# Kernel tuning notes

Hardware: AMD Instinct MI355X
Metric: run time of the kernel (lower is better)

The kernel has to match this reference:

```python
import jax, jax.numpy as jnp
import numpy as np

N = 100_000      # nodes
E = 3_000_000    # edges
G = 256          # graphs in batch
F_IN = 64        # num_features
NHID = 32


def setup_inputs() -> dict:
    key = jax.random.key(0)
    ks = jax.random.split(key, 12)
    x = jax.random.normal(ks[0], (N, F_IN), dtype=jnp.float32)
    edge_index = jax.random.randint(ks[1], (2, E), 0, N, dtype=jnp.int32)
    batch = jnp.sort(jax.random.randint(ks[2], (N,), 0, G, dtype=jnp.int32))
    # disjoint edge partitions used as integer index arrays (as in the torch code)
    perm = jax.random.permutation(ks[3], E).astype(jnp.int32)
    third = E // 3
    known_mask = perm[:third]
    unk_mask = perm[third:2 * third]
    obs_mask = perm[2 * third:]
    msg_weights = jax.random.normal(ks[4], (3,), dtype=jnp.float32)
    emb_W = jax.random.normal(ks[5], (F_IN - 1, 63), dtype=jnp.float32) * 0.1
    emb_b = jnp.zeros((63,), jnp.float32)
    gcn_W = jax.random.normal(ks[6], (64, NHID), dtype=jnp.float32) * 0.1
    gcn_b = jnp.zeros((NHID,), jnp.float32)
    fc1_W = jax.random.normal(ks[7], (NHID, NHID), dtype=jnp.float32) * 0.1
    fc1_b = jnp.zeros((NHID,), jnp.float32)
    out_W = jax.random.normal(ks[8], (NHID, 1), dtype=jnp.float32) * 0.1
    out_b = jnp.zeros((1,), jnp.float32)
    return dict(x=x, edge_index=edge_index, batch=batch, known_mask=known_mask,
                unk_mask=unk_mask, obs_mask=obs_mask, msg_weights=msg_weights,
                emb_W=emb_W, emb_b=emb_b, gcn_W=gcn_W, gcn_b=gcn_b,
                fc1_W=fc1_W, fc1_b=fc1_b, out_W=out_W, out_b=out_b)


def reference(x, edge_index, batch, known_mask, unk_mask, obs_mask,
              msg_weights, emb_W, emb_b, gcn_W, gcn_b,
              fc1_W, fc1_b, out_W, out_b):
    n_nodes = x.shape[0]
    n_edges = edge_index.shape[1]
    # edge weights from softmaxed message-type params (disjoint index sets)
    sp = jax.nn.softmax(msg_weights)
    ew = jnp.ones((n_edges,), x.dtype)
    ew = ew.at[known_mask].set(sp[0]).at[unk_mask].set(sp[1]).at[obs_mask].set(sp[2])
    # feature embed: keep col 0, embed the remaining 63 -> 63, concat to 64
    h = jnp.concatenate([x[:, :1], x[:, 1:] @ emb_W + emb_b], axis=1)  # [N,64]
    # GCNConv: add self-loops (weight 1), symmetric normalization
    loops = jnp.arange(n_nodes, dtype=edge_index.dtype)
    row = jnp.concatenate([edge_index[0], loops])
    col = jnp.concatenate([edge_index[1], loops])
    w = jnp.concatenate([ew, jnp.ones((n_nodes,), ew.dtype)])
    deg = jax.ops.segment_sum(w, col, num_segments=n_nodes)
    dinv = jnp.where(deg > 0, jax.lax.rsqrt(deg), 0.0)
    norm = dinv[row] * w * dinv[col]                   # [E+N]
    hW = h @ gcn_W                                     # [N,nhid]
    msg = norm[:, None] * hW[row]                      # gather + scale
    agg = jax.ops.segment_sum(msg, col, num_segments=n_nodes) + gcn_b
    hg = jax.nn.relu(agg)                              # dropout = identity (eval)
    pooled = jax.ops.segment_sum(hg, batch, num_segments=G)  # global_add_pool
    z = jax.nn.relu(pooled @ fc1_W + fc1_b)
    return z @ out_W + out_b                           # [G,1]
```

## Files before the change

kernel.cpp:

```cpp
#include <hip/hip_runtime.h>
#include <hip/hip_fp16.h>
#include <stdint.h>


#define BLK 256
#define NCHUNK 512
#define MAXNB 1600
#define ENTCAP 2560

__global__ void kA1(const int* __restrict__ col, int* __restrict__ cnt,
                    int n_edges, int NB,
                    const int* __restrict__ km, const int* __restrict__ um,
                    const int* __restrict__ om, int s0, int s1, int s2,
                    uint8_t* __restrict__ ewc) {
    __shared__ int lh[MAXNB];
    int t = threadIdx.x;
    if (blockIdx.x < NCHUNK) {
        int c = blockIdx.x;
        for (int b = t; b < NB; b += BLK) lh[b] = 0;
        __syncthreads();
        int chunk = (n_edges + NCHUNK - 1) / NCHUNK;
        int e0 = c * chunk, e1 = min(e0 + chunk, n_edges);
        for (int e = e0 + t; e < e1; e += BLK) atomicAdd(&lh[col[e] >> 6], 1);
        __syncthreads();
        for (int b = t; b < NB; b += BLK) cnt[(size_t)c * NB + b] = lh[b];
    } else {
        int m = blockIdx.x - NCHUNK;
        int sl = m & 7, g = m >> 3;
        int per = (n_edges + 7) >> 3;
        int elo = sl * per, ehi = min(elo + per, n_edges);
        int total = s0 + s1 + s2;
        int chunk = (total + 31) / 32;
        int i0 = g * chunk, i1 = min(i0 + chunk, total);
        for (int i = i0 + t; i < i1; i += BLK) {
            int e; uint8_t cls;
            if (i < s0)           { e = km[i];           cls = 0; }
            else if (i < s0 + s1) { e = um[i - s0];      cls = 1; }
            else                  { e = om[i - s0 - s1]; cls = 2; }
            if (e >= elo && e < ehi) ewc[e] = cls;
        }
    }
}

__global__ void kB2(const int* __restrict__ cnt, int* __restrict__ offTT,
                    int* __restrict__ tot, int NB) {
    __shared__ int tile[NCHUNK * 16];
    __shared__ int segs[16][17];
    int t = threadIdx.x;
    int b0 = blockIdx.x * 16;
    for (int idx = t; idx < NCHUNK * 16; idx += BLK) {
        int c = idx >> 4, b = idx & 15;
        tile[idx] = (b0 + b < NB) ? cnt[(size_t)c * NB + b0 + b] : 0;
    }
    __syncthreads();
    int b = t & 15, seg = t >> 4;
    int psum = 0;
#pragma unroll
    for (int k = 0; k < 32; ++k) psum += tile[(seg * 32 + k) * 16 + b];
    segs[seg][b] = psum;
    __syncthreads();
    int ex = 0;
    for (int ss = 0; ss < seg; ++ss) ex += segs[ss][b];
    int run = ex;
#pragma unroll
    for (int k = 0; k < 32; ++k) {
        int c = seg * 32 + k;
        if (b0 + b < NB) offTT[(size_t)c * NB + b0 + b] = run;
        run += tile[c * 16 + b];
    }
    if (seg == 15 && b0 + b < NB) tot[b0 + b] = run;
}

__global__ void kBase3(const int* __restrict__ tot, int* __restrict__ base_, int NB,
                       const float* __restrict__ emb_W, const float* __restrict__ emb_b,
                       const float* __restrict__ gcn_W,
                       float* __restrict__ Wfull, float* __restrict__ hWbias) {
    int t = threadIdx.x;
    if (blockIdx.x < 8) {
        int k = blockIdx.x * 8 + (t >> 5), j = t & 31;
        float acc;
        if (k == 0) {
            acc = gcn_W[j];
        } else {
            int m = k - 1;
            acc = 0.0f;
#pragma unroll 9
            for (int tt = 0; tt < 63; ++tt)
                acc += emb_W[m * 63 + tt] * gcn_W[(1 + tt) * 32 + j];
        }
        Wfull[k * 32 + j] = acc;
        if (blockIdx.x == 0 && t < 32) {
            float bacc = 0.0f;
            for (int tt = 0; tt < 63; ++tt)
                bacc += emb_b[tt] * gcn_W[(1 + tt) * 32 + t];
            hWbias[t] = bacc;
        }
    } else {
        __shared__ int s[BLK];
        const int K = 7;
        int v[K]; int sum = 0;
#pragma unroll
        for (int k = 0; k < K; ++k) {
            int i = t * K + k;
            v[k] = (i < NB) ? tot[i] : 0;
            sum += v[k];
        }
        s[t] = sum; __syncthreads();
        for (int st = 1; st < BLK; st <<= 1) {
            int x = (t >= st) ? s[t - st] : 0;
            __syncthreads(); s[t] += x; __syncthreads();
        }
        int ex = (t == 0) ? 0 : s[t - 1];
#pragma unroll
        for (int k = 0; k < K; ++k) {
            int i = t * K + k;
            if (i < NB) base_[i] = ex;
            ex += v[k];
        }
        if (t == BLK - 1) base_[NB] = s[BLK - 1];
    }
}

__global__ void kC_scatter(const int* __restrict__ row, const int* __restrict__ col,
                           const uint8_t* __restrict__ ewc, const int* __restrict__ base_,
                           const int* __restrict__ offTT, int* __restrict__ csrB,
                           int n_edges, int NB, int nbs) {
    __shared__ int cur[200];
    int sl = blockIdx.x & 7, c = blockIdx.x >> 3, t = threadIdx.x;
    int b0 = sl * nbs, b1 = min(b0 + nbs, NB);
    const int* offrow = offTT + (size_t)c * NB;
    for (int b = b0 + t; b < b1; b += BLK)
        cur[b - b0] = base_[b] + offrow[b];
    __syncthreads();
    int chunk = (n_edges + NCHUNK - 1) / NCHUNK;
    int e0 = c * chunk, e1 = min(e0 + chunk, n_edges);
    for (int e = e0 + t; e < e1; e += BLK) {
        int cc = col[e]; int b = cc >> 6;
        if (b >= b0 && b < b1) {
            int pos = atomicAdd(&cur[b - b0], 1);
            csrB[pos] = ((cc & 63) << 19) | (row[e] << 2) | (ewc[e] & 3);
        }
    }
}

__global__ void k4f_gemm(const float* __restrict__ x, const float* __restrict__ Wfull,
                         const float* __restrict__ hWbias, const int* __restrict__ base_,
                         const int* __restrict__ csrB, const float* __restrict__ mw,
                         __half* __restrict__ hWs, int n_nodes) {
    __shared__ float Wl[64 * 32];
    __shared__ float xs[64 * 64];
    __shared__ int ct4[256];
    __shared__ float dv[64];
    int b = blockIdx.x, t = threadIdx.x;
    for (int idx = t; idx < 2048; idx += BLK) Wl[idx] = Wfull[idx];
    if (t < 256) ct4[t] = 0;
    int rowBase = b * 64;
    for (int idx = t; idx < 4096; idx += BLK) {
        int r = rowBase + (idx >> 6);
        xs[idx] = (r < n_nodes) ? x[(size_t)r * 64 + (idx & 63)] : 0.0f;
    }
    __syncthreads();
    int p0 = base_[b], p1 = base_[b + 1];
    for (int p = p0 + t; p < p1; p += BLK) {
        int e = csrB[p];
        atomicAdd(&ct4[((e >> 19) << 2) | (e & 3)], 1);
    }
    __syncthreads();
    if (t < 64) {
        float a = mw[0], bb = mw[1], c3 = mw[2];
        float m = fmaxf(a, fmaxf(bb, c3));
        float ea = __expf(a - m), eb = __expf(bb - m), ec = __expf(c3 - m);
        float inv = 1.0f / (ea + eb + ec);
        float deg = (ea * inv) * (float)ct4[t * 4]
                  + (eb * inv) * (float)ct4[t * 4 + 1]
                  + (ec * inv) * (float)ct4[t * 4 + 2]
                  + (float)ct4[t * 4 + 3]
                  + 1.0f;
        dv[t] = rsqrtf(deg);
    }
    __syncthreads();
    int j = t & 31, lr = t >> 5;
#pragma unroll
    for (int k8 = 0; k8 < 8; ++k8) {
        int r = lr + 8 * k8;
        int n = rowBase + r;
        if (n < n_nodes) {
            float acc = hWbias[j];
#pragma unroll
            for (int k = 0; k < 64; ++k)
                acc += xs[r * 64 + k] * Wl[k * 32 + j];
            hWs[(size_t)n * 32 + j] = __float2half(dv[r] * acc);
        }
    }
}

__global__ void kD_gather(const int* __restrict__ base_, const int* __restrict__ csrB,
                          const __half2* __restrict__ hws2,
                          const float* __restrict__ mw, const float* __restrict__ gcn_b,
                          const int* __restrict__ batch, float* __restrict__ pooled,
                          int n_nodes) {
    __shared__ int ent[ENTCAP];
    __shared__ float res[64 * 33];
    __shared__ int ct4[256];
    __shared__ int ct[64], st[64], cur[64];
    __shared__ float dl[64], gb[32];
    __shared__ int bl[64];
    int b = blockIdx.x, t = threadIdx.x;
    if (t < 256) ct4[t] = 0;
    if (t < 64) {
        int n = b * 64 + t;
        bl[t] = (n < n_nodes) ? batch[n] : -1;
    }
    if (t < 32) gb[t] = gcn_b[t];
    __syncthreads();
    int p0 = base_[b], p1 = base_[b + 1];
    int m = min(p1 - p0, ENTCAP);
    int p1c = p0 + m;
    for (int p = p0 + t; p < p1c; p += BLK) {
        int e = csrB[p];
        atomicAdd(&ct4[((e >> 19) << 2) | (e & 3)], 1);
    }
    __syncthreads();
    float a = mw[0], bb = mw[1], c3 = mw[2];
    float mx = fmaxf(a, fmaxf(bb, c3));
    float ea = __expf(a - mx), eb = __expf(bb - mx), ec = __expf(c3 - mx);
    float inv = 1.0f / (ea + eb + ec);
    float w0 = ea * inv, w1 = eb * inv, w2 = ec * inv;
    if (t < 64) {
        int c0 = ct4[t * 4], c1 = ct4[t * 4 + 1], c2 = ct4[t * 4 + 2], c33 = ct4[t * 4 + 3];
        ct[t] = c0 + c1 + c2 + c33;
        dl[t] = rsqrtf(w0 * (float)c0 + w1 * (float)c1 + w2 * (float)c2
                       + (float)c33 + 1.0f);
    }
    __syncthreads();
    if (t < 64) st[t] = ct[t];
    __syncthreads();
    for (int off = 1; off < 64; off <<= 1) {
        int v = (t < 64 && t >= off) ? st[t - off] : 0;
        __syncthreads();
        if (t < 64) st[t] += v;
        __syncthreads();
    }
    if (t < 64) { st[t] -= ct[t]; cur[t] = st[t]; }
    __syncthreads();
    for (int p = p0 + t; p < p1c; p += BLK) {
        int e = csrB[p];
        int pos = atomicAdd(&cur[e >> 19], 1);
        ent[pos] = e;
    }
    __syncthreads();
    int grp = t >> 4, j2 = t & 15;
#pragma unroll
    for (int idx = 0; idx < 4; ++idx) {
        int lc = grp + 16 * idx;
        int n = b * 64 + lc;
        float rx = 0.0f, ry = 0.0f;
        if (n < n_nodes) {
            int s = st[lc], end = s + ct[lc];
            float ax = 0.0f, ay = 0.0f;
            int p = s;
            for (; p + 8 <= end; p += 8) {
                int e0 = ent[p],     e1 = ent[p + 1], e2 = ent[p + 2], e3 = ent[p + 3];
                int e4 = ent[p + 4], e5 = ent[p + 5], e6 = ent[p + 6], e7 = ent[p + 7];
                __half2 h0 = hws2[(size_t)((e0 >> 2) & 0x1FFFF) * 16 + j2];
                __half2 h1 = hws2[(size_t)((e1 >> 2) & 0x1FFFF) * 16 + j2];
                __half2 h2 = hws2[(size_t)((e2 >> 2) & 0x1FFFF) * 16 + j2];
                __half2 h3 = hws2[(size_t)((e3 >> 2) & 0x1FFFF) * 16 + j2];
                __half2 h4 = hws2[(size_t)((e4 >> 2) & 0x1FFFF) * 16 + j2];
                __half2 h5 = hws2[(size_t)((e5 >> 2) & 0x1FFFF) * 16 + j2];
                __half2 h6 = hws2[(size_t)((e6 >> 2) & 0x1FFFF) * 16 + j2];
                __half2 h7 = hws2[(size_t)((e7 >> 2) & 0x1FFFF) * 16 + j2];
                float f0 = ((e0 & 3) == 0) ? w0 : (((e0 & 3) == 1) ? w1 : w2);
                float f1 = ((e1 & 3) == 0) ? w0 : (((e1 & 3) == 1) ? w1 : w2);
                float f2 = ((e2 & 3) == 0) ? w0 : (((e2 & 3) == 1) ? w1 : w2);
                float f3 = ((e3 & 3) == 0) ? w0 : (((e3 & 3) == 1) ? w1 : w2);
                float f4 = ((e4 & 3) == 0) ? w0 : (((e4 & 3) == 1) ? w1 : w2);
                float f5 = ((e5 & 3) == 0) ? w0 : (((e5 & 3) == 1) ? w1 : w2);
                float f6 = ((e6 & 3) == 0) ? w0 : (((e6 & 3) == 1) ? w1 : w2);
                float f7 = ((e7 & 3) == 0) ? w0 : (((e7 & 3) == 1) ? w1 : w2);
                float2 g0 = __half22float2(h0), g1 = __half22float2(h1);
                float2 g2 = __half22float2(h2), g3 = __half22float2(h3);
                float2 g4 = __half22float2(h4), g5 = __half22float2(h5);
                float2 g6 = __half22float2(h6), g7 = __half22float2(h7);
                ax += f0 * g0.x + f1 * g1.x + f2 * g2.x + f3 * g3.x
                    + f4 * g4.x + f5 * g5.x + f6 * g6.x + f7 * g7.x;
                ay += f0 * g0.y + f1 * g1.y + f2 * g2.y + f3 * g3.y
                    + f4 * g4.y + f5 * g5.y + f6 * g6.y + f7 * g7.y;
            }
            for (; p < end; ++p) {
                int e0 = ent[p];
                __half2 h0 = hws2[(size_t)((e0 >> 2) & 0x1FFFF) * 16 + j2];
                float f0 = ((e0 & 3) == 0) ? w0 : (((e0 & 3) == 1) ? w1 : w2);
                float2 g0 = __half22float2(h0);
                ax += f0 * g0.x; ay += f0 * g0.y;
            }
            float2 self = __half22float2(hws2[(size_t)n * 16 + j2]);
            float di = dl[lc];
            rx = fmaxf(di * (ax + self.x) + gb[2 * j2], 0.0f);
            ry = fmaxf(di * (ay + self.y) + gb[2 * j2 + 1], 0.0f);
        }
        res[lc * 33 + 2 * j2]     = rx;
        res[lc * 33 + 2 * j2 + 1] = ry;
    }
    __syncthreads();
    if (t < 32) {
        int j = t;
        float sum = 0.0f; int g0 = bl[0];
        for (int lc = 0; lc < 64; ++lc) {
            if (bl[lc] < 0) break;
            float val = res[lc * 33 + j];
            if (bl[lc] != g0) { atomicAdd(&pooled[g0 * 32 + j], sum); sum = 0.0f; g0 = bl[lc]; }
            sum += val;
        }
        if (g0 >= 0) atomicAdd(&pooled[g0 * 32 + j], sum);
    }
}

__global__ void k7_head(const float* __restrict__ pooled, const float* __restrict__ fc1_W,
                        const float* __restrict__ fc1_b, const float* __restrict__ out_W,
                        const float* __restrict__ out_b, float* __restrict__ out,
                        int n_graphs) {
    __shared__ float Wl[32 * 32];
    __shared__ float bl[32];
    __shared__ float owl[32];
    int t = threadIdx.x;
    for (int idx = t; idx < 1024; idx += BLK) Wl[idx] = fc1_W[idx];
    if (t < 32) { bl[t] = fc1_b[t]; owl[t] = out_W[t]; }
    __syncthreads();
    if (t < n_graphs) {
        float p[32];
#pragma unroll
        for (int k = 0; k < 32; ++k) p[k] = pooled[t * 32 + k];
        float acc = 0.0f;
        for (int j = 0; j < 32; ++j) {
            float z = bl[j];
#pragma unroll
            for (int k = 0; k < 32; ++k) z += p[k] * Wl[k * 32 + j];
            z = fmaxf(z, 0.0f);
            acc += z * owl[j];
        }
        out[t] = acc + out_b[0];
    }
}

static inline size_t align_up(size_t v, size_t a) { return (v + a - 1) & ~(a - 1); }

extern "C" void kernel_launch(void* const* d_in, const int* in_sizes, int n_in,
                              void* d_out, int out_size, void* d_ws, size_t ws_size,
                              hipStream_t stream) {
    const float* x     = (const float*)d_in[0];
    const int*   ei    = (const int*)d_in[1];
    const int*   batch = (const int*)d_in[2];
    const int*   km    = (const int*)d_in[3];
    const int*   um    = (const int*)d_in[4];
    const int*   om    = (const int*)d_in[5];
    const float* mw    = (const float*)d_in[6];
    const float* emb_W = (const float*)d_in[7];
    const float* emb_b = (const float*)d_in[8];
    const float* gcn_W = (const float*)d_in[9];
    const float* gcn_b = (const float*)d_in[10];
    const float* fc1_W = (const float*)d_in[11];
    const float* fc1_b = (const float*)d_in[12];
    const float* out_W = (const float*)d_in[13];
    const float* out_b = (const float*)d_in[14];

    const int n_nodes  = in_sizes[0] / 64;
    const int n_edges  = in_sizes[1] / 2;
    const int s0 = in_sizes[3], s1 = in_sizes[4], s2 = in_sizes[5];
    const int n_graphs = out_size;

    const int* row = ei;
    const int* col = ei + n_edges;

    const int NB  = (n_nodes + 63) >> 6;
    const int NGB = (NB + 15) / 16;
    const int nbs = (NB + 7) / 8;

    char* base = (char*)d_ws;
    float*   pooled = (float*)base;   base += (size_t)n_graphs * 32 * 4;
    int*     cnt    = (int*)base;     base += (size_t)NCHUNK * NB * 4;
    int*     offTT  = (int*)base;     base += (size_t)NCHUNK * NB * 4;
    int*     tot    = (int*)base;     base += (size_t)NB * 4;
    int*     base_  = (int*)base;     base += (size_t)(NB + 1) * 4;
    float*   Wfull  = (float*)base;   base += 2048 * 4;
    float*   hWbias = (float*)base;   base += 32 * 4;
    uint8_t* ewc    = (uint8_t*)base; base += align_up((size_t)n_edges, 64);
    int*     csrB   = (int*)base;     base += (size_t)n_edges * 4;
    base = (char*)align_up((size_t)base, 64);
    __half*  hWs    = (__half*)base;  base += (size_t)n_nodes * 32 * 2;

    hipMemsetAsync(pooled, 0, (size_t)n_graphs * 32 * 4, stream);

    kA1<<<NCHUNK + 256, BLK, 0, stream>>>(col, cnt, n_edges, NB,
                                          km, um, om, s0, s1, s2, ewc);
    kB2<<<NGB, BLK, 0, stream>>>(cnt, offTT, tot, NB);
    kBase3<<<9, BLK, 0, stream>>>(tot, base_, NB, emb_W, emb_b, gcn_W, Wfull, hWbias);
    kC_scatter<<<NCHUNK * 8, BLK, 0, stream>>>(row, col, ewc, base_, offTT, csrB,
                                               n_edges, NB, nbs);
    k4f_gemm<<<NB, BLK, 0, stream>>>(x, Wfull, hWbias, base_, csrB, mw, hWs, n_nodes);
    kD_gather<<<NB, BLK, 0, stream>>>(base_, csrB, (const __half2*)hWs, mw,
                                      gcn_b, batch, pooled, n_nodes);
    k7_head<<<1, BLK, 0, stream>>>(pooled, fc1_W, fc1_b, out_W, out_b, (float*)d_out, n_graphs);
}
```

Measured before the change: 339.2 us.

## Bucket mask indices by edge slice before writing edge-class bytes

The old mask pass had each of 256 blocks scan a 1/32 share of all mask indices and write only those falling in its 1/8 edge slice, so every index was read 8 times. Now each block reads its share once, counts indices per slice, reserves space with global atomics, and writes packed (edge<<2|class) entries into per-slice buckets stored in the csrB buffer. A new kernel then scatters the bytes slice by slice to keep writes localized. This adds a launch, atomics and an extra round trip through the staging buffer, which relies on csrB being free until kC_scatter runs.

```diff
diff --git a/kernel.cpp b/kernel.cpp
--- a/kernel.cpp
+++ b/kernel.cpp
@@ -12,10 +12,10 @@
                     int n_edges, int NB,
                     const int* __restrict__ km, const int* __restrict__ um,
                     const int* __restrict__ om, int s0, int s1, int s2,
-                    uint8_t* __restrict__ ewc) {
-    __shared__ int lh[MAXNB];
+                    int* __restrict__ gcur, int* __restrict__ mbuf, int per) {
     int t = threadIdx.x;
     if (blockIdx.x < NCHUNK) {
+        __shared__ int lh[MAXNB];
         int c = blockIdx.x;
         for (int b = t; b < NB; b += BLK) lh[b] = 0;
         __syncthreads();
@@ -25,20 +25,48 @@
         __syncthreads();
         for (int b = t; b < NB; b += BLK) cnt[(size_t)c * NB + b] = lh[b];
     } else {
+        __shared__ int bcnt[8], bbase[8];
         int m = blockIdx.x - NCHUNK;
-        int sl = m & 7, g = m >> 3;
-        int per = (n_edges + 7) >> 3;
-        int elo = sl * per, ehi = min(elo + per, n_edges);
         int total = s0 + s1 + s2;
-        int chunk = (total + 31) / 32;
-        int i0 = g * chunk, i1 = min(i0 + chunk, total);
+        int chunk = (total + 255) / 256;
+        int i0 = m * chunk, i1 = min(i0 + chunk, total);
+        if (t < 8) bcnt[t] = 0;
+        __syncthreads();
         for (int i = i0 + t; i < i1; i += BLK) {
-            int e; uint8_t cls;
+            int e;
+            if (i < s0)           e = km[i];
+            else if (i < s0 + s1) e = um[i - s0];
+            else                  e = om[i - s0 - s1];
+            atomicAdd(&bcnt[min(e / per, 7)], 1);
+        }
+        __syncthreads();
+        if (t < 8) {
+            bbase[t] = atomicAdd(&gcur[t], bcnt[t]);
+            bcnt[t] = 0;
+        }
+        __syncthreads();
+        for (int i = i0 + t; i < i1; i += BLK) {
+            int e, cls;
             if (i < s0)           { e = km[i];           cls = 0; }
             else if (i < s0 + s1) { e = um[i - s0];      cls = 1; }
             else                  { e = om[i - s0 - s1]; cls = 2; }
-            if (e >= elo && e < ehi) ewc[e] = cls;
-        }
+            int b = min(e / per, 7);
+            int pos = bbase[b] + atomicAdd(&bcnt[b], 1);
+            mbuf[(size_t)b * per + pos] = (e << 2) | cls;
+        }
+    }
+}
+
+__global__ void kE_ewc(const int* __restrict__ gcur, const int* __restrict__ mbuf,
+                       uint8_t* __restrict__ ewc, int per) {
+    int sl = blockIdx.x & 7, k = blockIdx.x >> 3, t = threadIdx.x;
+    int cnt = gcur[sl];
+    int chunk = (cnt + 31) / 32;
+    int i0 = k * chunk, i1 = min(i0 + chunk, cnt);
+    const int* src = mbuf + (size_t)sl * per;
+    for (int i = i0 + t; i < i1; i += BLK) {
+        int pe = src[i];
+        ewc[pe >> 2] = (uint8_t)(pe & 3);
     }
 }
 
@@ -375,9 +403,11 @@
     const int NB  = (n_nodes + 63) >> 6;
     const int NGB = (NB + 15) / 16;
     const int nbs = (NB + 7) / 8;
+    const int per = (n_edges + 7) / 8;
 
     char* base = (char*)d_ws;
     float*   pooled = (float*)base;   base += (size_t)n_graphs * 32 * 4;
+    int*     gcur   = (int*)base;     base += 8 * 4;
     int*     cnt    = (int*)base;     base += (size_t)NCHUNK * NB * 4;
     int*     offTT  = (int*)base;     base += (size_t)NCHUNK * NB * 4;
     int*     tot    = (int*)base;     base += (size_t)NB * 4;
@@ -385,14 +415,17 @@
     float*   Wfull  = (float*)base;   base += 2048 * 4;
     float*   hWbias = (float*)base;   base += 32 * 4;
     uint8_t* ewc    = (uint8_t*)base; base += align_up((size_t)n_edges, 64);
-    int*     csrB   = (int*)base;     base += (size_t)n_edges * 4;
+    int*     csrB   = (int*)base;     base += (size_t)8 * per * 4;
     base = (char*)align_up((size_t)base, 64);
     __half*  hWs    = (__half*)base;  base += (size_t)n_nodes * 32 * 2;
 
-    hipMemsetAsync(pooled, 0, (size_t)n_graphs * 32 * 4, stream);
+    int* mbuf = csrB;
+
+    hipMemsetAsync(pooled, 0, (size_t)n_graphs * 32 * 4 + 8 * 4, stream);
 
     kA1<<<NCHUNK + 256, BLK, 0, stream>>>(col, cnt, n_edges, NB,
-                                          km, um, om, s0, s1, s2, ewc);
+                                          km, um, om, s0, s1, s2, gcur, mbuf, per);
+    kE_ewc<<<256, BLK, 0, stream>>>(gcur, mbuf, ewc, per);
     kB2<<<NGB, BLK, 0, stream>>>(cnt, offTT, tot, NB);
     kBase3<<<9, BLK, 0, stream>>>(tot, base_, NB, emb_W, emb_b, gcn_W, Wfull, hWbias);
     kC_scatter<<<NCHUNK * 8, BLK, 0, stream>>>(row, col, ewc, base_, offTT, csrB,
```

After: 318.6 us. 6.1% less time.
